# Optimization experiments

Hardware: AMD Instinct MI355X
Metric: run time of the kernel (lower is better)

The kernel has to match this reference:

```python
import jax, jax.numpy as jnp
import numpy as np

B, N, K, DIM = 512, 64, 12, 128


def setup_inputs() -> dict:
    key = jax.random.key(0)
    ks = jax.random.split(key, 8)
    return {
        "self_vectors": jax.random.normal(ks[0], (B, N, DIM), dtype=jnp.float32),
        "neighbor_vector": jax.random.normal(ks[1], (B, N, K, DIM), dtype=jnp.float32),
        "batch_size": B,
        "masks": jnp.ones((B, N), dtype=jnp.float32),
        "neighbor_weight": jax.random.uniform(ks[2], (B, N, K), dtype=jnp.float32),
        "extra_vector": jax.random.normal(ks[3], (B, N, DIM), dtype=jnp.float32),
        "w1": jax.random.normal(ks[4], (DIM + 1, DIM), dtype=jnp.float32) * 0.05,
        "w2": jax.random.normal(ks[5], (DIM, 1), dtype=jnp.float32) * 0.05,
        "w3": jax.random.normal(ks[6], (2 * DIM, DIM), dtype=jnp.float32) * 0.05,
    }


def reference(self_vectors, neighbor_vector, batch_size, masks, neighbor_weight,
              extra_vector, w1, w2, w3):
    dim = w3.shape[1]
    # [B,N,K,dim+1]: (extra tiled over K) * neighbors, concat edge weight
    feat = jnp.concatenate(
        [extra_vector[:, :, None, :] * neighbor_vector,
         neighbor_weight[..., None]], axis=-1)
    # attention logits: [B,N,K,dim] -> leaky_relu -> project to [B,N,K]
    alpha = jnp.einsum('bnkf,fd->bnkd', feat, w1)
    alpha = jax.nn.leaky_relu(alpha, negative_slope=0.2)
    alpha = jnp.einsum('bnkd,d->bnk', alpha, w2[:, 0])
    alpha = jax.nn.softmax(alpha, axis=-1)
    # weighted neighbor sum over K: [B,N,dim]
    agg = jnp.einsum('bnk,bnkd->bnd', alpha, neighbor_vector)
    # concat self + aggregated, transform, relu (dropout = identity at eval)
    out = jnp.concatenate([self_vectors, agg], axis=-1) @ w3
    out = out.reshape(batch_size, -1, dim)
    return jax.nn.relu(out)
```

## Files before the change

kernel.cpp:

```cpp
#include <hip/hip_runtime.h>

#define BN    32768
#define KNB   12
#define DIM   128

typedef __attribute__((ext_vector_type(8))) short bf16x8;
typedef __attribute__((ext_vector_type(4))) float f32x4;

__device__ inline unsigned short f2b(float x) {
    union { float f; unsigned u; } v; v.f = x;
    unsigned r = v.u + 0x7fffu + ((v.u >> 16) & 1u);
    return (unsigned short)(r >> 16);
}
__device__ inline float b2f(unsigned short s) {
    union { unsigned u; float f; } v; v.u = ((unsigned)s) << 16; return v.f;
}
__device__ inline unsigned pack2(float a, float b) {
    return (unsigned)f2b(a) | ((unsigned)f2b(b) << 16);
}

__global__ void prep_kernel(const float* __restrict__ w1, const float* __restrict__ w3,
                            unsigned short* __restrict__ w1f, unsigned short* __restrict__ w3f) {
    int idx = blockIdx.x * 256 + threadIdx.x;
    if (idx < 16384) {
        int j = idx & 7, lane = (idx >> 3) & 63, fi = idx >> 9;
        int nt = fi >> 2, ks = fi & 3;
        int k = ks * 32 + (lane >> 4) * 8 + j;
        int n = nt * 16 + (lane & 15);
        w1f[idx] = f2b(w1[k * DIM + n]);
    }
    if (idx < 32768) {
        int j = idx & 7, lane = (idx >> 3) & 63, fi = idx >> 9;
        int nt = fi >> 3, ks = fi & 7;
        int k = ks * 32 + (lane >> 4) * 8 + j;
        int n = nt * 16 + (lane & 15);
        w3f[idx] = f2b(w3[k * DIM + n]);
    }
}

#define T1   8
#define M1   96
#define LDA1 136

__global__ __launch_bounds__(256) void attn_mfma_kernel(
    const float* __restrict__ nbr_g,
    const float* __restrict__ nw_g,
    const float* __restrict__ ext_g,
    const float* __restrict__ w1,
    const float* __restrict__ w2,
    const unsigned short* __restrict__ w1f,
    unsigned short* __restrict__ aggb)
{
    __shared__ unsigned short featb[M1 * LDA1];
    __shared__ unsigned short nbrb[M1 * LDA1];
    __shared__ float logits[M1];
    __shared__ float wts[M1];

    const int tid  = threadIdx.x;
    const int lane = tid & 63;
    const int wv   = tid >> 6;
    const int bn0  = blockIdx.x * T1;

    const float4* nsrc  = (const float4*)(nbr_g + (size_t)bn0 * KNB * DIM);
    const float*  ebase = ext_g + (size_t)bn0 * DIM;
    #pragma unroll
    for (int i = 0; i < 12; ++i) {
        int f4  = tid + i * 256;
        int row = f4 >> 5;
        int c4  = f4 & 31;
        int node = row / 12;
        float4 nv = nsrc[f4];
        float4 ev = *(const float4*)(ebase + node * DIM + c4 * 4);
        uint2 pn; pn.x = pack2(nv.x, nv.y);           pn.y = pack2(nv.z, nv.w);
        uint2 pf; pf.x = pack2(nv.x * ev.x, nv.y * ev.y); pf.y = pack2(nv.z * ev.z, nv.w * ev.w);
        *(uint2*)&nbrb [row * LDA1 + c4 * 4] = pn;
        *(uint2*)&featb[row * LDA1 + c4 * 4] = pf;
    }
    __syncthreads();

    bf16x8 Bf[32];
    {
        const bf16x8* w1fv = (const bf16x8*)w1f;
        #pragma unroll
        for (int i = 0; i < 32; ++i) Bf[i] = w1fv[i * 64 + lane];
    }
    const int m    = lane & 15;
    const int quad = lane >> 4;
    float w2v[8], w1l[8];
    #pragma unroll
    for (int nt = 0; nt < 8; ++nt) {
        w2v[nt] = w2[nt * 16 + m];
        w1l[nt] = w1[DIM * DIM + nt * 16 + m];
    }

    for (int mt = wv; mt < 6; mt += 4) {
        const int rowbase = mt * 16 + quad * 4;
        float nwv[4];
        #pragma unroll
        for (int r = 0; r < 4; ++r) nwv[r] = nw_g[(size_t)bn0 * KNB + rowbase + r];
        float lp[4] = {0.f, 0.f, 0.f, 0.f};
        #pragma unroll
        for (int nt = 0; nt < 8; ++nt) {
            f32x4 acc = {0.f, 0.f, 0.f, 0.f};
            #pragma unroll
            for (int ks = 0; ks < 4; ++ks) {
                bf16x8 af = *(const bf16x8*)&featb[(mt * 16 + m) * LDA1 + ks * 32 + quad * 8];
                acc = __builtin_amdgcn_mfma_f32_16x16x32_bf16(af, Bf[nt * 4 + ks], acc, 0, 0, 0);
            }
            #pragma unroll
            for (int r = 0; r < 4; ++r) {
                float v = acc[r] + nwv[r] * w1l[nt];
                v = v > 0.f ? v : 0.2f * v;
                lp[r] += v * w2v[nt];
            }
        }
        #pragma unroll
        for (int r = 0; r < 4; ++r) {
            float v = lp[r];
            v += __shfl_xor(v, 1, 64); v += __shfl_xor(v, 2, 64);
            v += __shfl_xor(v, 4, 64); v += __shfl_xor(v, 8, 64);
            if (m == 0) logits[rowbase + r] = v;
        }
    }
    __syncthreads();

    if (tid < T1) {
        float mx = logits[tid * KNB];
        #pragma unroll
        for (int k = 1; k < KNB; ++k) mx = fmaxf(mx, logits[tid * KNB + k]);
        float s = 0.f; float e[KNB];
        #pragma unroll
        for (int k = 0; k < KNB; ++k) { e[k] = __expf(logits[tid * KNB + k] - mx); s += e[k]; }
        float inv = 1.f / s;
        #pragma unroll
        for (int k = 0; k < KNB; ++k) wts[tid * KNB + k] = e[k] * inv;
    }
    __syncthreads();

    {
        const int node = tid >> 5;
        const int dd   = (tid & 31) * 4;
        float a0 = 0.f, a1 = 0.f, a2 = 0.f, a3 = 0.f;
        #pragma unroll
        for (int k = 0; k < KNB; ++k) {
            float w = wts[node * KNB + k];
            uint2 pk = *(const uint2*)&nbrb[(node * KNB + k) * LDA1 + dd];
            a0 += w * b2f((unsigned short)(pk.x & 0xffff));
            a1 += w * b2f((unsigned short)(pk.x >> 16));
            a2 += w * b2f((unsigned short)(pk.y & 0xffff));
            a3 += w * b2f((unsigned short)(pk.y >> 16));
        }
        uint2 po; po.x = pack2(a0, a1); po.y = pack2(a2, a3);
        *(uint2*)&aggb[(size_t)(bn0 + node) * DIM + dd] = po;
    }
}

#define LDA2 264

__global__ __launch_bounds__(256) void out_mfma_kernel(
    const float* __restrict__ selfv,
    const unsigned short* __restrict__ aggb,
    const unsigned short* __restrict__ w3f,
    float* __restrict__ out)
{
    __shared__ unsigned short A[64 * LDA2];

    const int tid  = threadIdx.x;
    const int lane = tid & 63;
    const int wv   = tid >> 6;
    const int row0 = blockIdx.x * 64;

    const float4* ssrc = (const float4*)(selfv + (size_t)row0 * DIM);
    #pragma unroll
    for (int i = 0; i < 8; ++i) {
        int f4 = tid + i * 256;
        int r  = f4 >> 5, c4 = f4 & 31;
        float4 v = ssrc[f4];
        uint2 p; p.x = pack2(v.x, v.y); p.y = pack2(v.z, v.w);
        *(uint2*)&A[r * LDA2 + c4 * 4] = p;
    }
    const bf16x8* asrc = (const bf16x8*)(aggb + (size_t)row0 * DIM);
    #pragma unroll
    for (int i = 0; i < 4; ++i) {
        int idx = tid + i * 256;
        int r = idx >> 4, c8 = idx & 15;
        *(bf16x8*)&A[r * LDA2 + 128 + c8 * 8] = asrc[idx];
    }
    __syncthreads();

    bf16x8 Bf[16];
    {
        const bf16x8* w3fv = (const bf16x8*)w3f;
        #pragma unroll
        for (int i = 0; i < 16; ++i) {
            int nt = wv * 2 + (i >> 3), ks = i & 7;
            Bf[i] = w3fv[(nt * 8 + ks) * 64 + lane];
        }
    }
    const int m = lane & 15, quad = lane >> 4;

    for (int mt = 0; mt < 4; ++mt) {
        f32x4 acc0 = {0.f, 0.f, 0.f, 0.f}, acc1 = {0.f, 0.f, 0.f, 0.f};
        #pragma unroll
        for (int ks = 0; ks < 8; ++ks) {
            bf16x8 af = *(const bf16x8*)&A[(mt * 16 + m) * LDA2 + ks * 32 + quad * 8];
            acc0 = __builtin_amdgcn_mfma_f32_16x16x32_bf16(af, Bf[ks],     acc0, 0, 0, 0);
            acc1 = __builtin_amdgcn_mfma_f32_16x16x32_bf16(af, Bf[8 + ks], acc1, 0, 0, 0);
        }
        #pragma unroll
        for (int r = 0; r < 4; ++r) {
            int row = row0 + mt * 16 + quad * 4 + r;
            out[(size_t)row * DIM + wv * 32 + m]      = fmaxf(acc0[r], 0.f);
            out[(size_t)row * DIM + wv * 32 + 16 + m] = fmaxf(acc1[r], 0.f);
        }
    }
}

__global__ __launch_bounds__(128) void attn_agg_fb(
    const float* __restrict__ neighbor, const float* __restrict__ nw,
    const float* __restrict__ extra, const float* __restrict__ w1,
    const float* __restrict__ w2, float* __restrict__ agg)
{
    __shared__ float nbr_lds[2][KNB * DIM];
    const int wave = threadIdx.x >> 6, lane = threadIdx.x & 63;
    const int bn = blockIdx.x * 2 + wave;
    const float* nbr_gp = neighbor + (size_t)bn * (KNB * DIM);
    const float* ext_gp = extra + (size_t)bn * DIM;
    {
        const float4* s = (const float4*)nbr_gp;
        float4* d4 = (float4*)nbr_lds[wave];
        #pragma unroll
        for (int j = 0; j < 6; ++j) d4[lane + j * 64] = s[lane + j * 64];
    }
    __syncthreads();
    const int d0 = lane, d1 = lane + 64;
    float acc0[KNB], acc1[KNB];
    #pragma unroll
    for (int k = 0; k < KNB; ++k) { acc0[k] = 0.f; acc1[k] = 0.f; }
    const float* nbr_s = nbr_lds[wave];
    for (int f = 0; f < DIM; f += 4) {
        float4 ev = *(const float4*)(ext_gp + f);
        float q0[4], q1[4];
        #pragma unroll
        for (int j = 0; j < 4; ++j) {
            q0[j] = ((const float*)&ev)[j] * w1[(f + j) * DIM + d0];
            q1[j] = ((const float*)&ev)[j] * w1[(f + j) * DIM + d1];
        }
        #pragma unroll
        for (int k = 0; k < KNB; ++k) {
            float4 nv = *(const float4*)(nbr_s + k * DIM + f);
            acc0[k] += nv.x * q0[0] + nv.y * q0[1] + nv.z * q0[2] + nv.w * q0[3];
            acc1[k] += nv.x * q1[0] + nv.y * q1[1] + nv.z * q1[2] + nv.w * q1[3];
        }
    }
    const float* nwp = nw + (size_t)bn * KNB;
    const float w1t0 = w1[DIM * DIM + d0], w1t1 = w1[DIM * DIM + d1];
    const float w2a = w2[d0], w2b = w2[d1];
    float part[KNB];
    #pragma unroll
    for (int k = 0; k < KNB; ++k) {
        float a0 = acc0[k] + nwp[k] * w1t0, a1 = acc1[k] + nwp[k] * w1t1;
        a0 = a0 > 0.f ? a0 : 0.2f * a0; a1 = a1 > 0.f ? a1 : 0.2f * a1;
        part[k] = a0 * w2a + a1 * w2b;
    }
    #pragma unroll
    for (int k = 0; k < KNB; ++k) {
        float v = part[k];
        #pragma unroll
        for (int off = 32; off > 0; off >>= 1) v += __shfl_xor(v, off, 64);
        part[k] = v;
    }
    float mx = part[0];
    #pragma unroll
    for (int k = 1; k < KNB; ++k) mx = fmaxf(mx, part[k]);
    float s = 0.f;
    #pragma unroll
    for (int k = 0; k < KNB; ++k) { part[k] = __expf(part[k] - mx); s += part[k]; }
    const float inv = 1.f / s;
    float a0 = 0.f, a1 = 0.f;
    #pragma unroll
    for (int k = 0; k < KNB; ++k) {
        const float aw = part[k] * inv;
        a0 += aw * nbr_s[k * DIM + d0]; a1 += aw * nbr_s[k * DIM + d1];
    }
    agg[(size_t)bn * DIM + d0] = a0; agg[(size_t)bn * DIM + d1] = a1;
}

__global__ __launch_bounds__(256) void out_gemm_fb(
    const float* __restrict__ selfv, const float* __restrict__ agg,
    const float* __restrict__ w3, float* __restrict__ out)
{
    __shared__ float in_lds[64][256];
    const int row0 = blockIdx.x * 64, tid = threadIdx.x;
    for (int idx = tid; idx < 64 * 64; idx += 256) {
        const int r = idx >> 6, c4 = idx & 63;
        float4 v;
        if (c4 < 32) v = ((const float4*)(selfv + (size_t)(row0 + r) * DIM))[c4];
        else         v = ((const float4*)(agg + (size_t)(row0 + r) * DIM))[c4 - 32];
        ((float4*)in_lds[r])[c4] = v;
    }
    __syncthreads();
    const int d0 = tid & 63, rbase = (tid >> 6) * 16;
    float acc0[16], acc1[16];
    #pragma unroll
    for (int r = 0; r < 16; ++r) { acc0[r] = 0.f; acc1[r] = 0.f; }
    for (int f = 0; f < 256; f += 4) {
        float w3a[4], w3b[4];
        #pragma unroll
        for (int j = 0; j < 4; ++j) {
            w3a[j] = w3[(f + j) * DIM + d0]; w3b[j] = w3[(f + j) * DIM + d0 + 64];
        }
        #pragma unroll
        for (int r = 0; r < 16; ++r) {
            float4 iv = *(const float4*)(&in_lds[rbase + r][f]);
            acc0[r] += iv.x * w3a[0] + iv.y * w3a[1] + iv.z * w3a[2] + iv.w * w3a[3];
            acc1[r] += iv.x * w3b[0] + iv.y * w3b[1] + iv.z * w3b[2] + iv.w * w3b[3];
        }
    }
    #pragma unroll
    for (int r = 0; r < 16; ++r) {
        const size_t row = (size_t)(row0 + rbase + r);
        out[row * DIM + d0] = fmaxf(acc0[r], 0.f);
        out[row * DIM + d0 + 64] = fmaxf(acc1[r], 0.f);
    }
}

extern "C" void kernel_launch(void* const* d_in, const int* in_sizes, int n_in,
                              void* d_out, int out_size, void* d_ws, size_t ws_size,
                              hipStream_t stream) {
    const float* selfv    = (const float*)d_in[0];
    const float* neighbor = (const float*)d_in[1];
    const float* nw       = (const float*)d_in[4];
    const float* extra    = (const float*)d_in[5];
    const float* w1       = (const float*)d_in[6];
    const float* w2       = (const float*)d_in[7];
    const float* w3       = (const float*)d_in[8];
    float* out = (float*)d_out;

    const size_t need = (size_t)128 * 1024 + (size_t)BN * DIM * sizeof(unsigned short);
    if (ws_size >= need) {
        unsigned short* w1f  = (unsigned short*)d_ws;
        unsigned short* w3f  = (unsigned short*)((char*)d_ws + 32 * 1024);
        unsigned short* aggb = (unsigned short*)((char*)d_ws + 128 * 1024);
        prep_kernel<<<128, 256, 0, stream>>>(w1, w3, w1f, w3f);
        attn_mfma_kernel<<<BN / T1, 256, 0, stream>>>(neighbor, nw, extra, w1, w2, w1f, aggb);
        out_mfma_kernel<<<BN / 64, 256, 0, stream>>>(selfv, aggb, w3f, out);
    } else {
        attn_agg_fb<<<BN / 2, 128, 0, stream>>>(neighbor, nw, extra, w1, w2, out);
        out_gemm_fb<<<BN / 64, 256, 0, stream>>>(selfv, out, w3, out);
    }
}
```

Before: 345.9 us.

## Fuse attention aggregation and output GEMM into one kernel

```diff
diff --git a/kernel.cpp b/kernel.cpp
--- a/kernel.cpp
+++ b/kernel.cpp
@@ -41,15 +41,18 @@
 #define T1   8
 #define M1   96
 #define LDA1 136
-
-__global__ __launch_bounds__(256) void attn_mfma_kernel(
+#define LDA2 264
+
+__global__ __launch_bounds__(256) void fused_kernel(
     const float* __restrict__ nbr_g,
     const float* __restrict__ nw_g,
     const float* __restrict__ ext_g,
+    const float* __restrict__ selfv,
     const float* __restrict__ w1,
     const float* __restrict__ w2,
     const unsigned short* __restrict__ w1f,
-    unsigned short* __restrict__ aggb)
+    const unsigned short* __restrict__ w3f,
+    float* __restrict__ out)
 {
     __shared__ unsigned short featb[M1 * LDA1];
     __shared__ unsigned short nbrb[M1 * LDA1];
@@ -63,7 +66,7 @@
 
     const float4* nsrc  = (const float4*)(nbr_g + (size_t)bn0 * KNB * DIM);
     const float*  ebase = ext_g + (size_t)bn0 * DIM;
-    #pragma unroll
+    #pragma unroll 6
     for (int i = 0; i < 12; ++i) {
         int f4  = tid + i * 256;
         int row = f4 >> 5;
@@ -71,21 +74,16 @@
         int node = row / 12;
         float4 nv = nsrc[f4];
         float4 ev = *(const float4*)(ebase + node * DIM + c4 * 4);
-        uint2 pn; pn.x = pack2(nv.x, nv.y);           pn.y = pack2(nv.z, nv.w);
+        uint2 pn; pn.x = pack2(nv.x, nv.y);               pn.y = pack2(nv.z, nv.w);
         uint2 pf; pf.x = pack2(nv.x * ev.x, nv.y * ev.y); pf.y = pack2(nv.z * ev.z, nv.w * ev.w);
         *(uint2*)&nbrb [row * LDA1 + c4 * 4] = pn;
         *(uint2*)&featb[row * LDA1 + c4 * 4] = pf;
     }
     __syncthreads();
 
-    bf16x8 Bf[32];
-    {
-        const bf16x8* w1fv = (const bf16x8*)w1f;
-        #pragma unroll
-        for (int i = 0; i < 32; ++i) Bf[i] = w1fv[i * 64 + lane];
-    }
     const int m    = lane & 15;
     const int quad = lane >> 4;
+
     float w2v[8], w1l[8];
     #pragma unroll
     for (int nt = 0; nt < 8; ++nt) {
@@ -93,20 +91,25 @@
         w1l[nt] = w1[DIM * DIM + nt * 16 + m];
     }
 
+    const bf16x8* w1fv = (const bf16x8*)w1f;
     for (int mt = wv; mt < 6; mt += 4) {
         const int rowbase = mt * 16 + quad * 4;
         float nwv[4];
         #pragma unroll
         for (int r = 0; r < 4; ++r) nwv[r] = nw_g[(size_t)bn0 * KNB + rowbase + r];
+
+        bf16x8 af[4];
+        #pragma unroll
+        for (int ks = 0; ks < 4; ++ks)
+            af[ks] = *(const bf16x8*)&featb[(mt * 16 + m) * LDA1 + ks * 32 + quad * 8];
+
         float lp[4] = {0.f, 0.f, 0.f, 0.f};
         #pragma unroll
         for (int nt = 0; nt < 8; ++nt) {
             f32x4 acc = {0.f, 0.f, 0.f, 0.f};
             #pragma unroll
-            for (int ks = 0; ks < 4; ++ks) {
-                bf16x8 af = *(const bf16x8*)&featb[(mt * 16 + m) * LDA1 + ks * 32 + quad * 8];
-                acc = __builtin_amdgcn_mfma_f32_16x16x32_bf16(af, Bf[nt * 4 + ks], acc, 0, 0, 0);
-            }
+            for (int ks = 0; ks < 4; ++ks)
+                acc = __builtin_amdgcn_mfma_f32_16x16x32_bf16(af[ks], w1fv[(nt * 4 + ks) * 64 + lane], acc, 0, 0, 0);
             #pragma unroll
             for (int r = 0; r < 4; ++r) {
                 float v = acc[r] + nwv[r] * w1l[nt];
@@ -124,6 +127,15 @@
     }
     __syncthreads();
 
+    unsigned short* A2 = featb;
+
+    {
+        const int r  = tid >> 5;
+        const int c4 = tid & 31;
+        float4 v = *(const float4*)(selfv + (size_t)(bn0 + r) * DIM + c4 * 4);
+        uint2 p; p.x = pack2(v.x, v.y); p.y = pack2(v.z, v.w);
+        *(uint2*)&A2[r * LDA2 + c4 * 4] = p;
+    }
     if (tid < T1) {
         float mx = logits[tid * KNB];
         #pragma unroll
@@ -151,67 +163,30 @@
             a3 += w * b2f((unsigned short)(pk.y >> 16));
         }
         uint2 po; po.x = pack2(a0, a1); po.y = pack2(a2, a3);
-        *(uint2*)&aggb[(size_t)(bn0 + node) * DIM + dd] = po;
-    }
-}
-
-#define LDA2 264
-
-__global__ __launch_bounds__(256) void out_mfma_kernel(
-    const float* __restrict__ selfv,
-    const unsigned short* __restrict__ aggb,
-    const unsigned short* __restrict__ w3f,
-    float* __restrict__ out)
-{
-    __shared__ unsigned short A[64 * LDA2];
-
-    const int tid  = threadIdx.x;
-    const int lane = tid & 63;
-    const int wv   = tid >> 6;
-    const int row0 = blockIdx.x * 64;
-
-    const float4* ssrc = (const float4*)(selfv + (size_t)row0 * DIM);
-    #pragma unroll
-    for (int i = 0; i < 8; ++i) {
-        int f4 = tid + i * 256;
-        int r  = f4 >> 5, c4 = f4 & 31;
-        float4 v = ssrc[f4];
-        uint2 p; p.x = pack2(v.x, v.y); p.y = pack2(v.z, v.w);
-        *(uint2*)&A[r * LDA2 + c4 * 4] = p;
-    }
-    const bf16x8* asrc = (const bf16x8*)(aggb + (size_t)row0 * DIM);
-    #pragma unroll
-    for (int i = 0; i < 4; ++i) {
-        int idx = tid + i * 256;
-        int r = idx >> 4, c8 = idx & 15;
-        *(bf16x8*)&A[r * LDA2 + 128 + c8 * 8] = asrc[idx];
-    }
-    __syncthreads();
-
-    bf16x8 Bf[16];
+        *(uint2*)&A2[node * LDA2 + 128 + dd] = po;
+    }
+    __syncthreads();
+
     {
         const bf16x8* w3fv = (const bf16x8*)w3f;
-        #pragma unroll
-        for (int i = 0; i < 16; ++i) {
-            int nt = wv * 2 + (i >> 3), ks = i & 7;
-            Bf[i] = w3fv[(nt * 8 + ks) * 64 + lane];
-        }
-    }
-    const int m = lane & 15, quad = lane >> 4;
-
-    for (int mt = 0; mt < 4; ++mt) {
-        f32x4 acc0 = {0.f, 0.f, 0.f, 0.f}, acc1 = {0.f, 0.f, 0.f, 0.f};
-        #pragma unroll
-        for (int ks = 0; ks < 8; ++ks) {
-            bf16x8 af = *(const bf16x8*)&A[(mt * 16 + m) * LDA2 + ks * 32 + quad * 8];
-            acc0 = __builtin_amdgcn_mfma_f32_16x16x32_bf16(af, Bf[ks],     acc0, 0, 0, 0);
-            acc1 = __builtin_amdgcn_mfma_f32_16x16x32_bf16(af, Bf[8 + ks], acc1, 0, 0, 0);
-        }
-        #pragma unroll
-        for (int r = 0; r < 4; ++r) {
-            int row = row0 + mt * 16 + quad * 4 + r;
-            out[(size_t)row * DIM + wv * 32 + m]      = fmaxf(acc0[r], 0.f);
-            out[(size_t)row * DIM + wv * 32 + 16 + m] = fmaxf(acc1[r], 0.f);
+        bf16x8 af2[8];
+        #pragma unroll
+        for (int ks = 0; ks < 8; ++ks)
+            af2[ks] = *(const bf16x8*)&A2[m * LDA2 + ks * 32 + quad * 8];
+
+        #pragma unroll
+        for (int t = 0; t < 2; ++t) {
+            const int nt = wv * 2 + t;
+            f32x4 acc = {0.f, 0.f, 0.f, 0.f};
+            #pragma unroll
+            for (int ks = 0; ks < 8; ++ks)
+                acc = __builtin_amdgcn_mfma_f32_16x16x32_bf16(af2[ks], w3fv[(nt * 8 + ks) * 64 + lane], acc, 0, 0, 0);
+            #pragma unroll
+            for (int r = 0; r < 4; ++r) {
+                const int rl = quad * 4 + r;
+                if (rl < T1)
+                    out[(size_t)(bn0 + rl) * DIM + nt * 16 + m] = fmaxf(acc[r], 0.f);
+            }
         }
     }
 }
@@ -337,14 +312,12 @@
     const float* w3       = (const float*)d_in[8];
     float* out = (float*)d_out;
 
-    const size_t need = (size_t)128 * 1024 + (size_t)BN * DIM * sizeof(unsigned short);
-    if (ws_size >= need) {
-        unsigned short* w1f  = (unsigned short*)d_ws;
-        unsigned short* w3f  = (unsigned short*)((char*)d_ws + 32 * 1024);
-        unsigned short* aggb = (unsigned short*)((char*)d_ws + 128 * 1024);
+    if (ws_size >= (size_t)96 * 1024) {
+        unsigned short* w1f = (unsigned short*)d_ws;
+        unsigned short* w3f = (unsigned short*)((char*)d_ws + 32 * 1024);
         prep_kernel<<<128, 256, 0, stream>>>(w1, w3, w1f, w3f);
-        attn_mfma_kernel<<<BN / T1, 256, 0, stream>>>(neighbor, nw, extra, w1, w2, w1f, aggb);
-        out_mfma_kernel<<<BN / 64, 256, 0, stream>>>(selfv, aggb, w3f, out);
+        fused_kernel<<<BN / T1, 256, 0, stream>>>(neighbor, nw, extra, selfv,
+                                                  w1, w2, w1f, w3f, out);
     } else {
         attn_agg_fb<<<BN / 2, 128, 0, stream>>>(neighbor, nw, extra, w1, w2, out);
         out_gemm_fb<<<BN / 64, 256, 0, stream>>>(selfv, out, w3, out);
```

After: 350.2 us. Within noise of the previous version (+1.2%).
